# Kernel tuning notes

Measured on AMD Instinct MI355X. Metric: run time of the kernel, lower is better.

The kernel has to match this reference:

```python
import jax, jax.numpy as jnp
import numpy as np

B, F, E = 1024, 1024, 256      # batch, flat_shape (mobilenet), embedding_size
L1, L2, L3 = 16, 8, 32         # level1 classes, level2 classes per branch, level3 classes per leaf
NE3 = L1 * L2                  # 128 leaf (level-3) classifier heads


def setup_inputs() -> dict:
    key = jax.random.key(0)
    ks = jax.random.split(key, 10)
    w = lambda k, shape: (jax.random.normal(k, shape, jnp.float32) * 0.02)
    return {
        "features_x": jax.random.normal(ks[0], (B, F), jnp.float32),
        "features_y": jax.random.normal(ks[1], (B, F), jnp.float32),
        # level-1 head: Linear(F->E, no bias) + LayerNorm + ReLU + Linear(E->L1)
        "l1_W1": w(ks[2], (F, E)),
        "l1_g": jnp.ones((E,), jnp.float32), "l1_b": jnp.zeros((E,), jnp.float32),
        "l1_W2": w(ks[3], (E, L1)), "l1_b2": jnp.zeros((L1,), jnp.float32),
        # level-2 heads (one per level-1 class), stacked on a leading expert axis
        "l2_W1": w(ks[4], (L1, F, E)),
        "l2_g": jnp.ones((L1, E), jnp.float32), "l2_b": jnp.zeros((L1, E), jnp.float32),
        "l2_W2": w(ks[5], (L1, E, L2)), "l2_b2": jnp.zeros((L1, L2), jnp.float32),
        # level-3 heads (flattened [level1][level2] -> NE3 experts)
        "l3_W1": w(ks[6], (NE3, F, E)),
        "l3_g": jnp.ones((NE3, E), jnp.float32), "l3_b": jnp.zeros((NE3, E), jnp.float32),
        "l3_W2": w(ks[7], (NE3, E, L3)), "l3_b2": jnp.zeros((NE3, L3), jnp.float32),
    }


def _ln(h, g, b, eps=1e-5):
    m = jnp.mean(h, axis=-1, keepdims=True)
    v = jnp.mean(jnp.square(h - m), axis=-1, keepdims=True)
    return (h - m) * jax.lax.rsqrt(v + eps) * g + b


def reference(features_x, features_y,
              l1_W1, l1_g, l1_b, l1_W2, l1_b2,
              l2_W1, l2_g, l2_b, l2_W2, l2_b2,
              l3_W1, l3_g, l3_b, l3_W2, l3_b2):
    # Dropout is identity in eval mode.
    x, y = features_x, features_y
    rows = jnp.arange(x.shape[0])

    # level 1: single head on x
    h1 = jax.nn.relu(_ln(x @ l1_W1, l1_g, l1_b))
    logits1 = h1 @ l1_W2 + l1_b2                                # [B, L1]
    idx1 = jnp.argmax(logits1, axis=-1)                         # argmax(softmax) == argmax

    # level 2: routed head on 0.6*x + 0.4*y; compute all L1 heads batched, gather selected
    ft = 0.6 * x + 0.4 * y
    h2 = jax.nn.relu(_ln(jnp.einsum('bf,efh->beh', ft, l2_W1), l2_g, l2_b))  # [B, L1, E]
    logits2_all = jnp.einsum('beh,ehc->bec', h2, l2_W2) + l2_b2              # [B, L1, L2]
    logits2 = logits2_all[rows, idx1]                                        # [B, L2]
    idx2 = jnp.argmax(logits2, axis=-1)

    # level 3: doubly-routed head on x; flat expert index = idx1*L2 + idx2
    eidx = idx1 * logits2.shape[-1] + idx2
    h3 = jax.nn.relu(_ln(jnp.einsum('bf,efh->beh', x, l3_W1), l3_g, l3_b))   # [B, NE3, E]
    logits3_all = jnp.einsum('beh,ehc->bec', h3, l3_W2) + l3_b2              # [B, NE3, L3]
    logits3 = logits3_all[rows, eidx]                                        # [B, L3]

    # uniform class counts => pad_sequence is a no-op
    return (logits1, logits2, logits3)
```

## Files before the change

### kernel.cpp

```cpp
#include <hip/hip_runtime.h>

#define B_   1024
#define F_   1024
#define E_   256
#define NL1  16
#define NL2  8
#define NL3  32

__device__ __forceinline__ float b2f(unsigned short u) {
    union { unsigned int i; float f; } v;
    v.i = ((unsigned int)u) << 16;
    return v.f;
}

__device__ __forceinline__ unsigned short f2b(float f) {
    union { float f; unsigned int i; } v;
    v.f = f;
    unsigned int x = v.i;
    x += 0x7fffu + ((x >> 16) & 1u);
    return (unsigned short)(x >> 16);
}

__device__ __forceinline__ float ld1(const void* p, size_t i, int bf) {
    return bf ? b2f(((const unsigned short*)p)[i]) : ((const float*)p)[i];
}

__device__ __forceinline__ const void* eoff(const void* p, size_t elems, int bf) {
    return bf ? (const void*)((const unsigned short*)p + elems)
              : (const void*)((const float*)p + elems);
}

__device__ void head_one_row(
    const float* in,
    const void* W1, const void* g, const void* b,
    const void* W2, const void* b2, int NC, int bf,
    float* hn, float* red_s, float* red_ss, float* lg, int t)
{
    float acc = 0.0f;
    if (bf) {
        const unsigned short* W = (const unsigned short*)W1;
        for (int f = 0; f < F_; ++f) acc += in[f] * b2f(W[f * E_ + t]);
    } else {
        const float* W = (const float*)W1;
        for (int f = 0; f < F_; ++f) acc += in[f] * W[f * E_ + t];
    }

    red_s[t]  = acc;
    red_ss[t] = acc * acc;
    __syncthreads();
    for (int s = 128; s > 0; s >>= 1) {
        if (t < s) {
            red_s[t]  += red_s[t + s];
            red_ss[t] += red_ss[t + s];
        }
        __syncthreads();
    }
    float m    = red_s[0] * (1.0f / E_);
    float var  = red_ss[0] * (1.0f / E_) - m * m;
    float rstd = rsqrtf(var + 1e-5f);

    float v = (acc - m) * rstd * ld1(g, t, bf) + ld1(b, t, bf);
    hn[t] = fmaxf(v, 0.0f);
    __syncthreads();

    if (t < NC) {
        float a = ld1(b2, t, bf);
        if (bf) {
            const unsigned short* W = (const unsigned short*)W2;
            for (int e = 0; e < E_; ++e) a += hn[e] * b2f(W[e * NC + t]);
        } else {
            const float* W = (const float*)W2;
            for (int e = 0; e < E_; ++e) a += hn[e] * W[e * NC + t];
        }
        lg[t] = a;
    }
    __syncthreads();
}

__global__ void dtype_sniff_kernel(const unsigned int* l1g_words, int* flag) {
    if (threadIdx.x == 0 && blockIdx.x == 0) {
        *flag = (l1g_words[0] == 0x3F803F80u) ? 1 : 0;
    }
}

__global__ void MultiLevelClassifier_26491358282059_kernel(
    const void* x, const void* y,
    const void* l1W1, const void* l1g, const void* l1b,
    const void* l1W2, const void* l1b2,
    const void* l2W1, const void* l2g, const void* l2b,
    const void* l2W2, const void* l2b2,
    const void* l3W1, const void* l3g, const void* l3b,
    const void* l3W2, const void* l3b2,
    void* out, const int* flagp)
{
    __shared__ float xs[F_];
    __shared__ float fs[F_];
    __shared__ float hn[E_];
    __shared__ float red_s[E_];
    __shared__ float red_ss[E_];
    __shared__ float lg[NL3];
    __shared__ int   sel;

    const int t   = threadIdx.x;
    const int row = blockIdx.x;
    const int bf  = *flagp;

    for (int i = t; i < F_; i += 256) {
        float xv = ld1(x, (size_t)row * F_ + i, bf);
        float yv = ld1(y, (size_t)row * F_ + i, bf);
        xs[i] = xv;
        fs[i] = 0.6f * xv + 0.4f * yv;
    }
    __syncthreads();

    head_one_row(xs, l1W1, l1g, l1b, l1W2, l1b2, NL1, bf,
                 hn, red_s, red_ss, lg, t);
    if (t < NL1) {
        size_t o = (size_t)row * NL1 + t;
        if (bf) ((unsigned short*)out)[o] = f2b(lg[t]);
        else    ((float*)out)[o] = lg[t];
    }
    if (t == 0) {
        float best = lg[0]; int bi = 0;
        for (int c = 1; c < NL1; ++c)
            if (lg[c] > best) { best = lg[c]; bi = c; }
        sel = bi;
    }
    __syncthreads();
    const int i1 = sel;
    __syncthreads();

    head_one_row(fs,
                 eoff(l2W1, (size_t)i1 * F_ * E_, bf),
                 eoff(l2g,  (size_t)i1 * E_, bf),
                 eoff(l2b,  (size_t)i1 * E_, bf),
                 eoff(l2W2, (size_t)i1 * E_ * NL2, bf),
                 eoff(l2b2, (size_t)i1 * NL2, bf), NL2, bf,
                 hn, red_s, red_ss, lg, t);
    if (t < NL2) {
        size_t o = (size_t)B_ * NL1 + (size_t)row * NL2 + t;
        if (bf) ((unsigned short*)out)[o] = f2b(lg[t]);
        else    ((float*)out)[o] = lg[t];
    }
    if (t == 0) {
        float best = lg[0]; int bi = 0;
        for (int c = 1; c < NL2; ++c)
            if (lg[c] > best) { best = lg[c]; bi = c; }
        sel = i1 * NL2 + bi;
    }
    __syncthreads();
    const int e3 = sel;
    __syncthreads();

    head_one_row(xs,
                 eoff(l3W1, (size_t)e3 * F_ * E_, bf),
                 eoff(l3g,  (size_t)e3 * E_, bf),
                 eoff(l3b,  (size_t)e3 * E_, bf),
                 eoff(l3W2, (size_t)e3 * E_ * NL3, bf),
                 eoff(l3b2, (size_t)e3 * NL3, bf), NL3, bf,
                 hn, red_s, red_ss, lg, t);
    if (t < NL3) {
        size_t o = (size_t)B_ * (NL1 + NL2) + (size_t)row * NL3 + t;
        if (bf) ((unsigned short*)out)[o] = f2b(lg[t]);
        else    ((float*)out)[o] = lg[t];
    }
}

extern "C" void kernel_launch(void* const* d_in, const int* in_sizes, int n_in,
                              void* d_out, int out_size, void* d_ws, size_t ws_size,
                              hipStream_t stream) {
    (void)in_sizes; (void)n_in; (void)out_size; (void)ws_size;

    int* flag = (int*)d_ws;

    dtype_sniff_kernel<<<1, 1, 0, stream>>>((const unsigned int*)d_in[3], flag);

    MultiLevelClassifier_26491358282059_kernel<<<B_, 256, 0, stream>>>(
        d_in[0], d_in[1],
        d_in[2], d_in[3], d_in[4], d_in[5], d_in[6],
        d_in[7], d_in[8], d_in[9], d_in[10], d_in[11],
        d_in[12], d_in[13], d_in[14], d_in[15], d_in[16],
        d_out, flag);
}
```

Measured before the change: 405.1 us.

## Split-K vectorized matvec per row, warp-shuffle LayerNorm, parallel second-layer reduction

Restructures each routed head's computation within a block. The F dimension is split across four wavefronts, and each lane computes four output columns using vector loads (float4/ushort4). Per-wave partial sums are combined through shared memory. LayerNorm statistics now use wavefront shuffles instead of a shared-memory tree, and the second linear layer spreads its work over all 256 threads with a reduction, replacing the earlier version that used only NC threads. The goal is more memory-level parallelism and wider loads on a weight-streaming, latency-bound kernel, at the cost of extra shared memory and some added synchronisation.

```diff
diff --git a/kernel.cpp b/kernel.cpp
--- a/kernel.cpp
+++ b/kernel.cpp
@@ -21,58 +21,99 @@
     return (unsigned short)(x >> 16);
 }
 
-__device__ __forceinline__ float ld1(const void* p, size_t i, int bf) {
-    return bf ? b2f(((const unsigned short*)p)[i]) : ((const float*)p)[i];
-}
-
-__device__ __forceinline__ const void* eoff(const void* p, size_t elems, int bf) {
-    return bf ? (const void*)((const unsigned short*)p + elems)
-              : (const void*)((const float*)p + elems);
-}
-
-__device__ void head_one_row(
-    const float* in,
+template<int NC>
+__device__ void head_row(
+    const float* __restrict__ in,
     const void* W1, const void* g, const void* b,
-    const void* W2, const void* b2, int NC, int bf,
-    float* hn, float* red_s, float* red_ss, float* lg, int t)
+    const void* W2, const void* b2v, int bf,
+    float* part,
+    float* hn,
+    float* red,
+    float* lg,
+    int t)
 {
-    float acc = 0.0f;
-    if (bf) {
-        const unsigned short* W = (const unsigned short*)W1;
-        for (int f = 0; f < F_; ++f) acc += in[f] * b2f(W[f * E_ + t]);
-    } else {
-        const float* W = (const float*)W1;
-        for (int f = 0; f < F_; ++f) acc += in[f] * W[f * E_ + t];
-    }
-
-    red_s[t]  = acc;
-    red_ss[t] = acc * acc;
-    __syncthreads();
-    for (int s = 128; s > 0; s >>= 1) {
-        if (t < s) {
-            red_s[t]  += red_s[t + s];
-            red_ss[t] += red_ss[t + s];
+    const int lane = t & 63;
+    const int grp  = t >> 6;
+    const int e0   = lane * 4;
+
+    float a0 = 0.f, a1 = 0.f, a2 = 0.f, a3 = 0.f;
+    if (bf) {
+        const unsigned short* W = (const unsigned short*)W1 + (size_t)grp * 256 * E_;
+        #pragma unroll 4
+        for (int i = 0; i < 256; ++i) {
+            ushort4 w = *(const ushort4*)(W + (size_t)i * E_ + e0);
+            float xv = in[grp * 256 + i];
+            a0 += xv * b2f(w.x);
+            a1 += xv * b2f(w.y);
+            a2 += xv * b2f(w.z);
+            a3 += xv * b2f(w.w);
         }
+    } else {
+        const float* W = (const float*)W1 + (size_t)grp * 256 * E_;
+        #pragma unroll 4
+        for (int i = 0; i < 256; ++i) {
+            float4 w = *(const float4*)(W + (size_t)i * E_ + e0);
+            float xv = in[grp * 256 + i];
+            a0 += xv * w.x; a1 += xv * w.y; a2 += xv * w.z; a3 += xv * w.w;
+        }
+    }
+    part[grp * E_ + e0 + 0] = a0;
+    part[grp * E_ + e0 + 1] = a1;
+    part[grp * E_ + e0 + 2] = a2;
+    part[grp * E_ + e0 + 3] = a3;
+    __syncthreads();
+
+    float h = part[0 * E_ + t] + part[1 * E_ + t] + part[2 * E_ + t] + part[3 * E_ + t];
+
+    float s = h, ss = h * h;
+    #pragma unroll
+    for (int o = 32; o > 0; o >>= 1) {
+        s  += __shfl_xor(s, o);
+        ss += __shfl_xor(ss, o);
+    }
+    if (lane == 0) { red[grp * 2 + 0] = s; red[grp * 2 + 1] = ss; }
+    __syncthreads();
+    float S  = red[0] + red[2] + red[4] + red[6];
+    float SS = red[1] + red[3] + red[5] + red[7];
+    float m    = S * (1.0f / E_);
+    float var  = SS * (1.0f / E_) - m * m;
+    float rstd = rsqrtf(var + 1e-5f);
+
+    float gv, bv;
+    if (bf) {
+        gv = b2f(((const unsigned short*)g)[t]);
+        bv = b2f(((const unsigned short*)b)[t]);
+    } else {
+        gv = ((const float*)g)[t];
+        bv = ((const float*)b)[t];
+    }
+    hn[t] = fmaxf((h - m) * rstd * gv + bv, 0.0f);
+    __syncthreads();
+
+    constexpr int G  = 256 / NC;
+    constexpr int CH = E_ / G;
+    const int c = t % NC;
+    const int j = t / NC;
+    float a = 0.f;
+    if (bf) {
+        const unsigned short* W = (const unsigned short*)W2;
+        #pragma unroll 4
+        for (int e = j * CH; e < j * CH + CH; ++e) a += hn[e] * b2f(W[(size_t)e * NC + c]);
+    } else {
+        const float* W = (const float*)W2;
+        #pragma unroll 4
+        for (int e = j * CH; e < j * CH + CH; ++e) a += hn[e] * W[(size_t)e * NC + c];
+    }
+    part[j * NC + c] = a;
+    __syncthreads();
+    #pragma unroll
+    for (int sr = G / 2; sr > 0; sr >>= 1) {
+        if (j < sr) part[j * NC + c] += part[(j + sr) * NC + c];
         __syncthreads();
     }
-    float m    = red_s[0] * (1.0f / E_);
-    float var  = red_ss[0] * (1.0f / E_) - m * m;
-    float rstd = rsqrtf(var + 1e-5f);
-
-    float v = (acc - m) * rstd * ld1(g, t, bf) + ld1(b, t, bf);
-    hn[t] = fmaxf(v, 0.0f);
-    __syncthreads();
-
     if (t < NC) {
-        float a = ld1(b2, t, bf);
-        if (bf) {
-            const unsigned short* W = (const unsigned short*)W2;
-            for (int e = 0; e < E_; ++e) a += hn[e] * b2f(W[e * NC + t]);
-        } else {
-            const float* W = (const float*)W2;
-            for (int e = 0; e < E_; ++e) a += hn[e] * W[e * NC + t];
-        }
-        lg[t] = a;
+        float bias = bf ? b2f(((const unsigned short*)b2v)[t]) : ((const float*)b2v)[t];
+        lg[t] = part[t] + bias;
     }
     __syncthreads();
 }
@@ -83,7 +124,7 @@
     }
 }
 
-__global__ void MultiLevelClassifier_26491358282059_kernel(
+__global__ __launch_bounds__(256) void MultiLevelClassifier_26491358282059_kernel(
     const void* x, const void* y,
     const void* l1W1, const void* l1g, const void* l1b,
     const void* l1W2, const void* l1b2,
@@ -95,9 +136,9 @@
 {
     __shared__ float xs[F_];
     __shared__ float fs[F_];
+    __shared__ float part[4 * E_];
     __shared__ float hn[E_];
-    __shared__ float red_s[E_];
-    __shared__ float red_ss[E_];
+    __shared__ float red[8];
     __shared__ float lg[NL3];
     __shared__ int   sel;
 
@@ -105,16 +146,27 @@
     const int row = blockIdx.x;
     const int bf  = *flagp;
 
-    for (int i = t; i < F_; i += 256) {
-        float xv = ld1(x, (size_t)row * F_ + i, bf);
-        float yv = ld1(y, (size_t)row * F_ + i, bf);
-        xs[i] = xv;
-        fs[i] = 0.6f * xv + 0.4f * yv;
-    }
-    __syncthreads();
-
-    head_one_row(xs, l1W1, l1g, l1b, l1W2, l1b2, NL1, bf,
-                 hn, red_s, red_ss, lg, t);
+    if (bf) {
+        ushort4 xv = ((const ushort4*)x)[(size_t)row * 256 + t];
+        ushort4 yv = ((const ushort4*)y)[(size_t)row * 256 + t];
+        float x0 = b2f(xv.x), x1 = b2f(xv.y), x2 = b2f(xv.z), x3 = b2f(xv.w);
+        xs[t * 4 + 0] = x0; xs[t * 4 + 1] = x1; xs[t * 4 + 2] = x2; xs[t * 4 + 3] = x3;
+        fs[t * 4 + 0] = 0.6f * x0 + 0.4f * b2f(yv.x);
+        fs[t * 4 + 1] = 0.6f * x1 + 0.4f * b2f(yv.y);
+        fs[t * 4 + 2] = 0.6f * x2 + 0.4f * b2f(yv.z);
+        fs[t * 4 + 3] = 0.6f * x3 + 0.4f * b2f(yv.w);
+    } else {
+        float4 xv = ((const float4*)x)[(size_t)row * 256 + t];
+        float4 yv = ((const float4*)y)[(size_t)row * 256 + t];
+        xs[t * 4 + 0] = xv.x; xs[t * 4 + 1] = xv.y; xs[t * 4 + 2] = xv.z; xs[t * 4 + 3] = xv.w;
+        fs[t * 4 + 0] = 0.6f * xv.x + 0.4f * yv.x;
+        fs[t * 4 + 1] = 0.6f * xv.y + 0.4f * yv.y;
+        fs[t * 4 + 2] = 0.6f * xv.z + 0.4f * yv.z;
+        fs[t * 4 + 3] = 0.6f * xv.w + 0.4f * yv.w;
+    }
+    __syncthreads();
+
+    head_row<NL1>(xs, l1W1, l1g, l1b, l1W2, l1b2, bf, part, hn, red, lg, t);
     if (t < NL1) {
         size_t o = (size_t)row * NL1 + t;
         if (bf) ((unsigned short*)out)[o] = f2b(lg[t]);
@@ -128,15 +180,20 @@
     }
     __syncthreads();
     const int i1 = sel;
-    __syncthreads();
-
-    head_one_row(fs,
-                 eoff(l2W1, (size_t)i1 * F_ * E_, bf),
-                 eoff(l2g,  (size_t)i1 * E_, bf),
-                 eoff(l2b,  (size_t)i1 * E_, bf),
-                 eoff(l2W2, (size_t)i1 * E_ * NL2, bf),
-                 eoff(l2b2, (size_t)i1 * NL2, bf), NL2, bf,
-                 hn, red_s, red_ss, lg, t);
+
+    {
+        const void* W1 = bf ? (const void*)((const unsigned short*)l2W1 + (size_t)i1 * F_ * E_)
+                            : (const void*)((const float*)l2W1 + (size_t)i1 * F_ * E_);
+        const void* g  = bf ? (const void*)((const unsigned short*)l2g + (size_t)i1 * E_)
+                            : (const void*)((const float*)l2g + (size_t)i1 * E_);
+        const void* b  = bf ? (const void*)((const unsigned short*)l2b + (size_t)i1 * E_)
+                            : (const void*)((const float*)l2b + (size_t)i1 * E_);
+        const void* W2 = bf ? (const void*)((const unsigned short*)l2W2 + (size_t)i1 * E_ * NL2)
+                            : (const void*)((const float*)l2W2 + (size_t)i1 * E_ * NL2);
+        const void* b2 = bf ? (const void*)((const unsigned short*)l2b2 + (size_t)i1 * NL2)
+                            : (const void*)((const float*)l2b2 + (size_t)i1 * NL2);
+        head_row<NL2>(fs, W1, g, b, W2, b2, bf, part, hn, red, lg, t);
+    }
     if (t < NL2) {
         size_t o = (size_t)B_ * NL1 + (size_t)row * NL2 + t;
         if (bf) ((unsigned short*)out)[o] = f2b(lg[t]);
@@ -150,15 +207,20 @@
     }
     __syncthreads();
     const int e3 = sel;
-    __syncthreads();
-
-    head_one_row(xs,
-                 eoff(l3W1, (size_t)e3 * F_ * E_, bf),
-                 eoff(l3g,  (size_t)e3 * E_, bf),
-                 eoff(l3b,  (size_t)e3 * E_, bf),
-                 eoff(l3W2, (size_t)e3 * E_ * NL3, bf),
-                 eoff(l3b2, (size_t)e3 * NL3, bf), NL3, bf,
-                 hn, red_s, red_ss, lg, t);
+
+    {
+        const void* W1 = bf ? (const void*)((const unsigned short*)l3W1 + (size_t)e3 * F_ * E_)
+                            : (const void*)((const float*)l3W1 + (size_t)e3 * F_ * E_);
+        const void* g  = bf ? (const void*)((const unsigned short*)l3g + (size_t)e3 * E_)
+                            : (const void*)((const float*)l3g + (size_t)e3 * E_);
+        const void* b  = bf ? (const void*)((const unsigned short*)l3b + (size_t)e3 * E_)
+                            : (const void*)((const float*)l3b + (size_t)e3 * E_);
+        const void* W2 = bf ? (const void*)((const unsigned short*)l3W2 + (size_t)e3 * E_ * NL3)
+                            : (const void*)((const float*)l3W2 + (size_t)e3 * E_ * NL3);
+        const void* b2 = bf ? (const void*)((const unsigned short*)l3b2 + (size_t)e3 * NL3)
+                            : (const void*)((const float*)l3b2 + (size_t)e3 * NL3);
+        head_row<NL3>(xs, W1, g, b, W2, b2, bf, part, hn, red, lg, t);
+    }
     if (t < NL3) {
         size_t o = (size_t)B_ * (NL1 + NL2) + (size_t)row * NL3 + t;
         if (bf) ((unsigned short*)out)[o] = f2b(lg[t]);
```

Measured after the change: 374.2 us. -7.6%, faster.
